# Performance work log

Hardware: AMD Instinct MI355X
Metric: run time of the kernel (lower is better)

## Reference

```python
import jax, jax.numpy as jnp
import numpy as np

N = 50000        # nodes
E = 1600000      # edges (before self loops)
IN = 256         # in_channels
C = 32           # hidden_channels (per head)
H = 4            # heads
OUT = 64         # out_channels
NEG_SLOPE = 0.2  # PyG GATConv default


def setup_inputs() -> dict:
    key = jax.random.key(0)
    ks = jax.random.split(key, 8)
    x = jax.random.normal(ks[0], (N, IN), dtype=jnp.float32)
    edge_index = jax.random.randint(ks[1], (2, E), 0, N, dtype=jnp.int64)
    s = 0.05
    W = jax.random.normal(ks[2], (IN, H * C), dtype=jnp.float32) * s
    att_src = jax.random.normal(ks[3], (H, C), dtype=jnp.float32) * s
    att_dst = jax.random.normal(ks[4], (H, C), dtype=jnp.float32) * s
    bias = jnp.zeros((H * C,), dtype=jnp.float32)
    lin_W = jax.random.normal(ks[5], (H * C, OUT), dtype=jnp.float32) * s
    lin_b = jnp.zeros((OUT,), dtype=jnp.float32)
    return {"x": x, "edge_index": edge_index, "W": W, "att_src": att_src,
            "att_dst": att_dst, "bias": bias, "lin_W": lin_W, "lin_b": lin_b}


def reference(x, edge_index, W, att_src, att_dst, bias, lin_W, lin_b):
    # Linear transform per head: [N, H, C]
    h = (x @ W).reshape(N, H, C)
    # Per-node attention halves (PyG GATConv): [N, H]
    a_src = jnp.einsum('nhc,hc->nh', h, att_src)
    a_dst = jnp.einsum('nhc,hc->nh', h, att_dst)
    # Add self loops (PyG default add_self_loops=True)
    loop = jnp.arange(N, dtype=edge_index.dtype)
    src = jnp.concatenate([edge_index[0], loop])  # message source j
    dst = jnp.concatenate([edge_index[1], loop])  # message target i
    # Edge attention logits: LeakyReLU(a_src[j] + a_dst[i])  -> [E+N, H]
    e = jax.nn.leaky_relu(a_src[src] + a_dst[dst], negative_slope=NEG_SLOPE)
    # Segment softmax over incoming edges of each destination node
    emax = jax.lax.stop_gradient(jax.ops.segment_max(e, dst, num_segments=N))
    emax = jnp.where(jnp.isfinite(emax), emax, 0.0)
    ex = jnp.exp(e - emax[dst])
    denom = jax.ops.segment_sum(ex, dst, num_segments=N)
    alpha = ex / denom[dst]  # [E+N, H]; self loops guarantee denom > 0
    # Weighted scatter-sum of source features: [N, H, C]
    msg = alpha[:, :, None] * h[src]
    agg = jax.ops.segment_sum(msg, dst, num_segments=N)
    out = agg.reshape(N, H * C) + bias  # concat heads + bias
    out = jax.nn.elu(out)
    return out @ lin_W + lin_b
```

## Files before the change

kernel.cpp:

```cpp
#include <hip/hip_runtime.h>
#include <cstdint>
#include <cstddef>

#define N_NODES 50000
#define N_EDGES 1600000
#define TOT_E   (N_EDGES + N_NODES)
#define IN_DIM  256
#define HC      128
#define NHEAD   4
#define OUT_DIM 64

#define SHIFT   7
#define BSZ     128
#define NBUK    ((N_NODES + BSZ - 1) / BSZ)
#define CHUNK   2048
#define EPT     8
#define NCHUNK  ((TOT_E + CHUNK - 1) / CHUNK)
#define CAP     6144

#define XPAD 264
#define HPAD 132

typedef __attribute__((ext_vector_type(8))) short bf16x8;
typedef __attribute__((ext_vector_type(4))) float f32x4;

static __device__ __forceinline__ uint16_t f2bf(float f) {
    uint32_t u = __float_as_uint(f);
    uint32_t r = (u + 0x7fffu + ((u >> 16) & 1u)) >> 16;
    return (uint16_t)r;
}
static __device__ __forceinline__ float bf_lo(uint32_t u) {
    return __uint_as_float(u << 16);
}
static __device__ __forceinline__ float bf_hi(uint32_t u) {
    return __uint_as_float(u & 0xffff0000u);
}

__global__ __launch_bounds__(256) void w2bf(const float* __restrict__ W,
                                            uint16_t* __restrict__ wt) {
    int idx = blockIdx.x * 256 + threadIdx.x;
    int n = idx >> 8, k = idx & 255;
    wt[idx] = f2bf(W[(size_t)k * HC + n]);
}

__global__ __launch_bounds__(256) void k1_mfma(const float* __restrict__ x,
                                               const uint16_t* __restrict__ wt,
                                               const float* __restrict__ att_src,
                                               const float* __restrict__ att_dst,
                                               uint16_t* __restrict__ hb,
                                               float* __restrict__ a_src,
                                               float* __restrict__ a_dst) {
    __shared__ char smem[64 * 528];
    __shared__ float att_s[HC], att_d[HC];
    uint16_t* xs = (uint16_t*)smem;
    float*    hs = (float*)smem;

    const int tid  = threadIdx.x;
    const int wave = tid >> 6;
    const int lane = tid & 63;
    const int m    = lane & 15;
    const int q    = lane >> 4;
    const int row0 = blockIdx.x * 64;

    if (tid < HC) { att_s[tid] = att_src[tid]; att_d[tid] = att_dst[tid]; }

    for (int i = tid * 4; i < 64 * IN_DIM; i += 1024) {
        int r = i >> 8, c = i & 255;
        int gr = row0 + r;
        float4 v = make_float4(0.f, 0.f, 0.f, 0.f);
        if (gr < N_NODES) v = *(const float4*)(x + (size_t)gr * IN_DIM + c);
        uint32_t lo = (uint32_t)f2bf(v.x) | ((uint32_t)f2bf(v.y) << 16);
        uint32_t hi = (uint32_t)f2bf(v.z) | ((uint32_t)f2bf(v.w) << 16);
        *(uint2*)(xs + r * XPAD + c) = make_uint2(lo, hi);
    }
    __syncthreads();

    f32x4 acc[8];
    #pragma unroll
    for (int t = 0; t < 8; ++t) acc[t] = (f32x4){0.f, 0.f, 0.f, 0.f};

    const int arow = wave * 16 + m;
    #pragma unroll
    for (int ks = 0; ks < IN_DIM; ks += 32) {
        bf16x8 a = *(const bf16x8*)(xs + arow * XPAD + ks + q * 8);
        #pragma unroll
        for (int t = 0; t < 8; ++t) {
            bf16x8 b = *(const bf16x8*)(wt + (size_t)(t * 16 + m) * IN_DIM + ks + q * 8);
            acc[t] = __builtin_amdgcn_mfma_f32_16x16x32_bf16(a, b, acc[t], 0, 0, 0);
        }
    }
    __syncthreads();

    #pragma unroll
    for (int t = 0; t < 8; ++t)
        #pragma unroll
        for (int r = 0; r < 4; ++r)
            hs[(wave * 16 + q * 4 + r) * HPAD + t * 16 + m] = acc[t][r];
    __syncthreads();

    for (int i = tid * 4; i < 64 * HC; i += 1024) {
        int r = i >> 7, c = i & 127;
        if (row0 + r < N_NODES) {
            float4 v = *(const float4*)(hs + r * HPAD + c);
            uint32_t lo = (uint32_t)f2bf(v.x) | ((uint32_t)f2bf(v.y) << 16);
            uint32_t hi = (uint32_t)f2bf(v.z) | ((uint32_t)f2bf(v.w) << 16);
            *(uint2*)(hb + (size_t)(row0 + r) * HC + c) = make_uint2(lo, hi);
        }
    }
    {
        int r = tid >> 2, hd = tid & 3;
        if (row0 + r < N_NODES) {
            float s = 0.f, d = 0.f;
            #pragma unroll
            for (int j = 0; j < 32; ++j) {
                float v = hs[r * HPAD + hd * 32 + j];
                s = fmaf(v, att_s[hd * 32 + j], s);
                d = fmaf(v, att_d[hd * 32 + j], d);
            }
            a_src[(row0 + r) * NHEAD + hd] = s;
            a_dst[(row0 + r) * NHEAD + hd] = d;
        }
    }
}

__global__ __launch_bounds__(256) void p3_bin(const int* __restrict__ ei,
                                              int* __restrict__ gcur,
                                              uint32_t* __restrict__ binned) {
    __shared__ int hist[NBUK];
    __shared__ int lcur[NBUK];
    const int tid = threadIdx.x;
    for (int i = tid; i < NBUK; i += 256) hist[i] = 0;
    __syncthreads();

    uint32_t wreg[EPT];
    const int base = blockIdx.x * CHUNK;
    #pragma unroll
    for (int k = 0; k < EPT; ++k) {
        int e = base + k * 256 + tid;
        uint32_t word = 0xFFFFFFFFu;
        if (e < TOT_E) {
            int src, dst;
            if (e < N_EDGES) { src = ei[e]; dst = ei[N_EDGES + e]; }
            else             { src = e - N_EDGES; dst = src; }
            int b = dst >> SHIFT;
            word = (uint32_t)src | ((uint32_t)(dst & (BSZ - 1)) << 16)
                 | ((uint32_t)b << 23);
            atomicAdd(&hist[b], 1);
        }
        wreg[k] = word;
    }
    __syncthreads();
    for (int i = tid; i < NBUK; i += 256) {
        int c = hist[i];
        lcur[i] = c ? atomicAdd(&gcur[i], c) : 0;
    }
    __syncthreads();
    #pragma unroll
    for (int k = 0; k < EPT; ++k) {
        uint32_t word = wreg[k];
        if (word != 0xFFFFFFFFu) {
            int b = (int)(word >> 23);
            int pos = atomicAdd(&lcur[b], 1);
            if (pos < CAP) binned[(size_t)b * CAP + pos] = word;
        }
    }
}

__global__ __launch_bounds__(512) void p4_csr(const uint32_t* __restrict__ binned,
                                              const int* __restrict__ gcur,
                                              int* __restrict__ rbeg,
                                              int* __restrict__ rend,
                                              int* __restrict__ csr_src) {
    __shared__ uint32_t ew[CAP];
    __shared__ int ncnt[BSZ];
    __shared__ int ncur[BSZ];
    __shared__ int wtot;
    const int b    = blockIdx.x;
    const int base = b * CAP;
    int cnt = gcur[b];
    if (cnt > CAP) cnt = CAP;
    const int tid  = threadIdx.x;

    if (tid < BSZ) ncnt[tid] = 0;
    __syncthreads();

    for (int i = tid; i < cnt; i += 512) {
        uint32_t word = binned[base + i];
        ew[i] = word;
        atomicAdd(&ncnt[(word >> 16) & (BSZ - 1)], 1);
    }
    __syncthreads();

    int v = 0, inc = 0;
    if (tid < BSZ) {
        v = ncnt[tid];
        inc = v;
        int lane = tid & 63;
        #pragma unroll
        for (int d = 1; d < 64; d <<= 1) {
            int t = __shfl_up(inc, d, 64);
            if (lane >= d) inc += t;
        }
        if (tid == 63) wtot = inc;
    }
    __syncthreads();
    if (tid < BSZ) {
        int ex = inc - v + ((tid >= 64) ? wtot : 0);
        int node = b * BSZ + tid;
        if (node < N_NODES) {
            rbeg[node] = base + ex;
            rend[node] = base + ex + v;
        }
        ncur[tid] = ex;
    }
    __syncthreads();

    for (int i = tid; i < cnt; i += 512) {
        uint32_t word = ew[i];
        int local = (word >> 16) & (BSZ - 1);
        int r = atomicAdd(&ncur[local], 1);
        csr_src[base + r] = (int)(word & 0xFFFFu);
    }
}

__global__ __launch_bounds__(64) void k6_agg(const uint32_t* __restrict__ hb32,
                                             const float* __restrict__ a_src,
                                             const float* __restrict__ a_dst,
                                             const int* __restrict__ rbeg,
                                             const int* __restrict__ rend,
                                             const int* __restrict__ csr_src,
                                             const float* __restrict__ bias,
                                             uint32_t* __restrict__ actb) {
    const int node = blockIdx.x;
    const int lane = threadIdx.x;
    const int head = lane >> 4;

    const float ad  = a_dst[node * NHEAD + head];
    const uint32_t* hbl = hb32 + lane;
    const float*    ash = a_src + head;

    int p   = rbeg[node];
    const int end = rend[node];

    float l = 0.f, acc0 = 0.f, acc1 = 0.f;

    for (; p + 4 <= end; p += 4) {
        int s0 = csr_src[p + 0];
        int s1 = csr_src[p + 1];
        int s2 = csr_src[p + 2];
        int s3 = csr_src[p + 3];
        float e0 = ash[s0 * NHEAD] + ad;
        float e1 = ash[s1 * NHEAD] + ad;
        float e2 = ash[s2 * NHEAD] + ad;
        float e3 = ash[s3 * NHEAD] + ad;
        uint32_t u0 = hbl[(size_t)s0 * 64];
        uint32_t u1 = hbl[(size_t)s1 * 64];
        uint32_t u2 = hbl[(size_t)s2 * 64];
        uint32_t u3 = hbl[(size_t)s3 * 64];
        e0 = fmaxf(e0, 0.2f * e0);
        e1 = fmaxf(e1, 0.2f * e1);
        e2 = fmaxf(e2, 0.2f * e2);
        e3 = fmaxf(e3, 0.2f * e3);
        float w0 = __expf(e0), w1 = __expf(e1);
        float w2 = __expf(e2), w3 = __expf(e3);
        l += (w0 + w1) + (w2 + w3);
        acc0 = fmaf(w0, bf_lo(u0), acc0);
        acc1 = fmaf(w0, bf_hi(u0), acc1);
        acc0 = fmaf(w1, bf_lo(u1), acc0);
        acc1 = fmaf(w1, bf_hi(u1), acc1);
        acc0 = fmaf(w2, bf_lo(u2), acc0);
        acc1 = fmaf(w2, bf_hi(u2), acc1);
        acc0 = fmaf(w3, bf_lo(u3), acc0);
        acc1 = fmaf(w3, bf_hi(u3), acc1);
    }
    for (; p < end; ++p) {
        int s = csr_src[p];
        float e = ash[s * NHEAD] + ad;
        e = fmaxf(e, 0.2f * e);
        float w = __expf(e);
        uint32_t u = hbl[(size_t)s * 64];
        l += w;
        acc0 = fmaf(w, bf_lo(u), acc0);
        acc1 = fmaf(w, bf_hi(u), acc1);
    }

    const int c0 = lane << 1;
    float inv = 1.f / l;
    float o0 = acc0 * inv + bias[c0];
    float o1 = acc1 * inv + bias[c0 + 1];
    o0 = (o0 > 0.f) ? o0 : (__expf(o0) - 1.f);
    o1 = (o1 > 0.f) ? o1 : (__expf(o1) - 1.f);
    actb[(size_t)node * 64 + lane] = (uint32_t)f2bf(o0) | ((uint32_t)f2bf(o1) << 16);
}

__global__ __launch_bounds__(512) void k7_out(const uint32_t* __restrict__ actb,
                                              const float* __restrict__ linW,
                                              const float* __restrict__ linb,
                                              float* __restrict__ out) {
    __shared__ float sW[HC * OUT_DIM];
    __shared__ float srow[32 * HC];
    const int tid   = threadIdx.x;
    const int node0 = blockIdx.x * 32;

    for (int i = tid * 4; i < HC * OUT_DIM; i += 512 * 4)
        *(float4*)(sW + i) = *(const float4*)(linW + i);
    {
        int i = tid * 4;
        int r = i >> 6, cw = i & 63;
        int node = node0 + r;
        uint4 v = make_uint4(0, 0, 0, 0);
        if (node < N_NODES) v = *(const uint4*)(actb + (size_t)node * 64 + cw);
        float* d = srow + r * HC + cw * 2;
        d[0] = bf_lo(v.x); d[1] = bf_hi(v.x);
        d[2] = bf_lo(v.y); d[3] = bf_hi(v.y);
        d[4] = bf_lo(v.z); d[5] = bf_hi(v.z);
        d[6] = bf_lo(v.w); d[7] = bf_hi(v.w);
    }
    __syncthreads();

    const int r    = tid >> 4;
    const int colb = (tid & 15) << 2;
    float4 acc = *(const float4*)(linb + colb);
    const float* rp = srow + r * HC;

    #pragma unroll
    for (int k = 0; k < HC; k += 4) {
        float4 xv = *(const float4*)(rp + k);
        float4 w0 = *(const float4*)(sW + (k + 0) * OUT_DIM + colb);
        float4 w1 = *(const float4*)(sW + (k + 1) * OUT_DIM + colb);
        float4 w2 = *(const float4*)(sW + (k + 2) * OUT_DIM + colb);
        float4 w3 = *(const float4*)(sW + (k + 3) * OUT_DIM + colb);
        acc.x += xv.x * w0.x; acc.x += xv.y * w1.x; acc.x += xv.z * w2.x; acc.x += xv.w * w3.x;
        acc.y += xv.x * w0.y; acc.y += xv.y * w1.y; acc.y += xv.z * w2.y; acc.y += xv.w * w3.y;
        acc.z += xv.x * w0.z; acc.z += xv.y * w1.z; acc.z += xv.z * w2.z; acc.z += xv.w * w3.z;
        acc.w += xv.x * w0.w; acc.w += xv.y * w1.w; acc.w += xv.z * w2.w; acc.w += xv.w * w3.w;
    }

    int node = node0 + r;
    if (node < N_NODES)
        *(float4*)(out + (size_t)node * OUT_DIM + colb) = acc;
}

extern "C" void kernel_launch(void* const* d_in, const int* in_sizes, int n_in,
                              void* d_out, int out_size, void* d_ws, size_t ws_size,
                              hipStream_t stream) {
    (void)in_sizes; (void)n_in; (void)out_size; (void)ws_size;
    const float* x       = (const float*)d_in[0];
    const int*   ei      = (const int*)d_in[1];
    const float* W       = (const float*)d_in[2];
    const float* att_src = (const float*)d_in[3];
    const float* att_dst = (const float*)d_in[4];
    const float* bias    = (const float*)d_in[5];
    const float* linW    = (const float*)d_in[6];
    const float* linb    = (const float*)d_in[7];
    float*       out     = (float*)d_out;

    char*  ws  = (char*)d_ws;
    size_t off = 0;
    auto alloc = [&](size_t bytes) -> void* {
        void* p = ws + off;
        off += (bytes + 255) & ~(size_t)255;
        return p;
    };
    uint16_t* hb     = (uint16_t*)alloc((size_t)N_NODES * HC * 2);
    uint16_t* wt     = (uint16_t*)alloc((size_t)HC * IN_DIM * 2);
    uint32_t* actb   = (uint32_t*)alloc((size_t)N_NODES * 64 * 4);
    float*    a_src  = (float*)alloc((size_t)N_NODES * NHEAD * 4);
    float*    a_dst  = (float*)alloc((size_t)N_NODES * NHEAD * 4);
    int*      gcur   = (int*)alloc((size_t)NBUK * 4);
    int*      rbeg   = (int*)alloc((size_t)N_NODES * 4);
    int*      rend   = (int*)alloc((size_t)N_NODES * 4);
    uint32_t* binned = (uint32_t*)alloc((size_t)NBUK * CAP * 4);
    int*      csr    = (int*)alloc((size_t)NBUK * CAP * 4);

    hipMemsetAsync(gcur, 0, (size_t)NBUK * 4, stream);

    w2bf<<<(HC * IN_DIM) / 256, 256, 0, stream>>>(W, wt);
    k1_mfma<<<(N_NODES + 63) / 64, 256, 0, stream>>>(x, wt, att_src, att_dst,
                                                     hb, a_src, a_dst);
    p3_bin<<<NCHUNK, 256, 0, stream>>>(ei, gcur, binned);
    p4_csr<<<NBUK, 512, 0, stream>>>(binned, gcur, rbeg, rend, csr);
    k6_agg<<<N_NODES, 64, 0, stream>>>((const uint32_t*)hb, a_src, a_dst,
                                       rbeg, rend, csr, bias, actb);
    k7_out<<<(N_NODES + 31) / 32, 512, 0, stream>>>(actb, linW, linb, out);
}
```

Measured before the change: 265.1 us.

## Fuse GEMM with edge binning and fold CSR build into aggregation

Folds the gcur memset into the weight conversion kernel and runs the MFMA projection and edge binning as two block ranges of one launch. The separate CSR kernel is removed: each aggregation block reads its bucket, keeps the edges for 32 destination nodes, counting-sorts them in shared memory, then aggregates with one wave per node in turn. This cuts launches and the global CSR write and read, but every bucket is scanned four times, and a quarter-bucket overflowing QCAP would silently drop edges.

```diff
diff --git a/kernel.cpp b/kernel.cpp
--- a/kernel.cpp
+++ b/kernel.cpp
@@ -17,9 +17,11 @@
 #define EPT     8
 #define NCHUNK  ((TOT_E + CHUNK - 1) / CHUNK)
 #define CAP     6144
+#define QCAP    1792
 
 #define XPAD 264
 #define HPAD 132
+#define K1_NB ((N_NODES + 63) / 64)
 
 typedef __attribute__((ext_vector_type(8))) short bf16x8;
 typedef __attribute__((ext_vector_type(4))) float f32x4;
@@ -37,260 +39,257 @@
 }
 
 __global__ __launch_bounds__(256) void w2bf(const float* __restrict__ W,
-                                            uint16_t* __restrict__ wt) {
+                                            uint16_t* __restrict__ wt,
+                                            int* __restrict__ gcur) {
     int idx = blockIdx.x * 256 + threadIdx.x;
     int n = idx >> 8, k = idx & 255;
     wt[idx] = f2bf(W[(size_t)k * HC + n]);
-}
-
-__global__ __launch_bounds__(256) void k1_mfma(const float* __restrict__ x,
-                                               const uint16_t* __restrict__ wt,
-                                               const float* __restrict__ att_src,
-                                               const float* __restrict__ att_dst,
-                                               uint16_t* __restrict__ hb,
-                                               float* __restrict__ a_src,
-                                               float* __restrict__ a_dst) {
+    if (idx < NBUK) gcur[idx] = 0;
+}
+
+__global__ __launch_bounds__(256) void k1p3(const float* __restrict__ x,
+                                            const uint16_t* __restrict__ wt,
+                                            const float* __restrict__ att_src,
+                                            const float* __restrict__ att_dst,
+                                            uint16_t* __restrict__ hb,
+                                            float* __restrict__ a_src,
+                                            float* __restrict__ a_dst,
+                                            const int* __restrict__ ei,
+                                            int* __restrict__ gcur,
+                                            uint32_t* __restrict__ binned) {
     __shared__ char smem[64 * 528];
     __shared__ float att_s[HC], att_d[HC];
-    uint16_t* xs = (uint16_t*)smem;
-    float*    hs = (float*)smem;
-
-    const int tid  = threadIdx.x;
+    const int tid = threadIdx.x;
+
+    if (blockIdx.x < K1_NB) {
+        uint16_t* xs = (uint16_t*)smem;
+        float*    hs = (float*)smem;
+        const int wave = tid >> 6;
+        const int lane = tid & 63;
+        const int m    = lane & 15;
+        const int q    = lane >> 4;
+        const int row0 = blockIdx.x * 64;
+
+        if (tid < HC) { att_s[tid] = att_src[tid]; att_d[tid] = att_dst[tid]; }
+
+        for (int i = tid * 4; i < 64 * IN_DIM; i += 1024) {
+            int r = i >> 8, c = i & 255;
+            int gr = row0 + r;
+            float4 v = make_float4(0.f, 0.f, 0.f, 0.f);
+            if (gr < N_NODES) v = *(const float4*)(x + (size_t)gr * IN_DIM + c);
+            uint32_t lo = (uint32_t)f2bf(v.x) | ((uint32_t)f2bf(v.y) << 16);
+            uint32_t hi = (uint32_t)f2bf(v.z) | ((uint32_t)f2bf(v.w) << 16);
+            *(uint2*)(xs + r * XPAD + c) = make_uint2(lo, hi);
+        }
+        __syncthreads();
+
+        f32x4 acc[8];
+        #pragma unroll
+        for (int t = 0; t < 8; ++t) acc[t] = (f32x4){0.f, 0.f, 0.f, 0.f};
+
+        const int arow = wave * 16 + m;
+        #pragma unroll
+        for (int ks = 0; ks < IN_DIM; ks += 32) {
+            bf16x8 a = *(const bf16x8*)(xs + arow * XPAD + ks + q * 8);
+            #pragma unroll
+            for (int t = 0; t < 8; ++t) {
+                bf16x8 b = *(const bf16x8*)(wt + (size_t)(t * 16 + m) * IN_DIM + ks + q * 8);
+                acc[t] = __builtin_amdgcn_mfma_f32_16x16x32_bf16(a, b, acc[t], 0, 0, 0);
+            }
+        }
+        __syncthreads();
+
+        #pragma unroll
+        for (int t = 0; t < 8; ++t)
+            #pragma unroll
+            for (int r = 0; r < 4; ++r)
+                hs[(wave * 16 + q * 4 + r) * HPAD + t * 16 + m] = acc[t][r];
+        __syncthreads();
+
+        for (int i = tid * 4; i < 64 * HC; i += 1024) {
+            int r = i >> 7, c = i & 127;
+            if (row0 + r < N_NODES) {
+                float4 v = *(const float4*)(hs + r * HPAD + c);
+                uint32_t lo = (uint32_t)f2bf(v.x) | ((uint32_t)f2bf(v.y) << 16);
+                uint32_t hi = (uint32_t)f2bf(v.z) | ((uint32_t)f2bf(v.w) << 16);
+                *(uint2*)(hb + (size_t)(row0 + r) * HC + c) = make_uint2(lo, hi);
+            }
+        }
+        {
+            int r = tid >> 2, hd = tid & 3;
+            if (row0 + r < N_NODES) {
+                float s = 0.f, d = 0.f;
+                #pragma unroll
+                for (int j = 0; j < 32; ++j) {
+                    float v = hs[r * HPAD + hd * 32 + j];
+                    s = fmaf(v, att_s[hd * 32 + j], s);
+                    d = fmaf(v, att_d[hd * 32 + j], d);
+                }
+                a_src[(row0 + r) * NHEAD + hd] = s;
+                a_dst[(row0 + r) * NHEAD + hd] = d;
+            }
+        }
+    } else {
+        int* hist = (int*)smem;
+        int* lcur = hist + NBUK;
+        for (int i = tid; i < NBUK; i += 256) hist[i] = 0;
+        __syncthreads();
+
+        uint32_t wreg[EPT];
+        const int base = (blockIdx.x - K1_NB) * CHUNK;
+        #pragma unroll
+        for (int k = 0; k < EPT; ++k) {
+            int e = base + k * 256 + tid;
+            uint32_t word = 0xFFFFFFFFu;
+            if (e < TOT_E) {
+                int src, dst;
+                if (e < N_EDGES) { src = ei[e]; dst = ei[N_EDGES + e]; }
+                else             { src = e - N_EDGES; dst = src; }
+                int b = dst >> SHIFT;
+                word = (uint32_t)src | ((uint32_t)(dst & (BSZ - 1)) << 16)
+                     | ((uint32_t)b << 23);
+                atomicAdd(&hist[b], 1);
+            }
+            wreg[k] = word;
+        }
+        __syncthreads();
+        for (int i = tid; i < NBUK; i += 256) {
+            int c = hist[i];
+            lcur[i] = c ? atomicAdd(&gcur[i], c) : 0;
+        }
+        __syncthreads();
+        #pragma unroll
+        for (int k = 0; k < EPT; ++k) {
+            uint32_t word = wreg[k];
+            if (word != 0xFFFFFFFFu) {
+                int b = (int)(word >> 23);
+                int pos = atomicAdd(&lcur[b], 1);
+                if (pos < CAP) binned[(size_t)b * CAP + pos] = word;
+            }
+        }
+    }
+}
+
+__global__ __launch_bounds__(256) void q4_agg(const uint32_t* __restrict__ binned,
+                                              const int* __restrict__ gcur,
+                                              const uint32_t* __restrict__ hb32,
+                                              const float* __restrict__ a_src,
+                                              const float* __restrict__ a_dst,
+                                              const float* __restrict__ bias,
+                                              uint32_t* __restrict__ actb) {
+    __shared__ uint32_t ewb[QCAP];
+    __shared__ uint32_t ew2[QCAP];
+    __shared__ int ncnt[32], nbeg[32], ncur[32];
+    __shared__ int tot;
+    const int b   = blockIdx.x >> 2;
+    const int sub = blockIdx.x & 3;
+    const int tid = threadIdx.x;
+
+    int cnt = gcur[b];
+    if (cnt > CAP) cnt = CAP;
+    if (tid == 0) tot = 0;
+    if (tid < 32) ncnt[tid] = 0;
+    __syncthreads();
+
+    const uint32_t* bb = binned + (size_t)b * CAP;
+    for (int i = tid; i < cnt; i += 256) {
+        uint32_t word = bb[i];
+        int dl = (word >> 16) & 127;
+        if ((dl >> 5) == sub) {
+            int pos = atomicAdd(&tot, 1);
+            if (pos < QCAP) ewb[pos] = word;
+            atomicAdd(&ncnt[dl & 31], 1);
+        }
+    }
+    __syncthreads();
+    int T = tot;
+    if (T > QCAP) T = QCAP;
+
+    if (tid < 32) {
+        int v = ncnt[tid];
+        int inc = v;
+        #pragma unroll
+        for (int d = 1; d < 32; d <<= 1) {
+            int t = __shfl_up(inc, d, 64);
+            if (tid >= d) inc += t;
+        }
+        nbeg[tid] = inc - v;
+        ncur[tid] = inc - v;
+    }
+    __syncthreads();
+    for (int i = tid; i < T; i += 256) {
+        uint32_t word = ewb[i];
+        int ln  = (word >> 16) & 31;
+        int pos = atomicAdd(&ncur[ln], 1);
+        ew2[pos] = word & 0xFFFFu;
+    }
+    __syncthreads();
+
     const int wave = tid >> 6;
     const int lane = tid & 63;
-    const int m    = lane & 15;
-    const int q    = lane >> 4;
-    const int row0 = blockIdx.x * 64;
-
-    if (tid < HC) { att_s[tid] = att_src[tid]; att_d[tid] = att_dst[tid]; }
-
-    for (int i = tid * 4; i < 64 * IN_DIM; i += 1024) {
-        int r = i >> 8, c = i & 255;
-        int gr = row0 + r;
-        float4 v = make_float4(0.f, 0.f, 0.f, 0.f);
-        if (gr < N_NODES) v = *(const float4*)(x + (size_t)gr * IN_DIM + c);
-        uint32_t lo = (uint32_t)f2bf(v.x) | ((uint32_t)f2bf(v.y) << 16);
-        uint32_t hi = (uint32_t)f2bf(v.z) | ((uint32_t)f2bf(v.w) << 16);
-        *(uint2*)(xs + r * XPAD + c) = make_uint2(lo, hi);
-    }
-    __syncthreads();
-
-    f32x4 acc[8];
-    #pragma unroll
-    for (int t = 0; t < 8; ++t) acc[t] = (f32x4){0.f, 0.f, 0.f, 0.f};
-
-    const int arow = wave * 16 + m;
-    #pragma unroll
-    for (int ks = 0; ks < IN_DIM; ks += 32) {
-        bf16x8 a = *(const bf16x8*)(xs + arow * XPAD + ks + q * 8);
-        #pragma unroll
-        for (int t = 0; t < 8; ++t) {
-            bf16x8 b = *(const bf16x8*)(wt + (size_t)(t * 16 + m) * IN_DIM + ks + q * 8);
-            acc[t] = __builtin_amdgcn_mfma_f32_16x16x32_bf16(a, b, acc[t], 0, 0, 0);
-        }
-    }
-    __syncthreads();
-
-    #pragma unroll
-    for (int t = 0; t < 8; ++t)
-        #pragma unroll
-        for (int r = 0; r < 4; ++r)
-            hs[(wave * 16 + q * 4 + r) * HPAD + t * 16 + m] = acc[t][r];
-    __syncthreads();
-
-    for (int i = tid * 4; i < 64 * HC; i += 1024) {
-        int r = i >> 7, c = i & 127;
-        if (row0 + r < N_NODES) {
-            float4 v = *(const float4*)(hs + r * HPAD + c);
-            uint32_t lo = (uint32_t)f2bf(v.x) | ((uint32_t)f2bf(v.y) << 16);
-            uint32_t hi = (uint32_t)f2bf(v.z) | ((uint32_t)f2bf(v.w) << 16);
-            *(uint2*)(hb + (size_t)(row0 + r) * HC + c) = make_uint2(lo, hi);
-        }
-    }
-    {
-        int r = tid >> 2, hd = tid & 3;
-        if (row0 + r < N_NODES) {
-            float s = 0.f, d = 0.f;
-            #pragma unroll
-            for (int j = 0; j < 32; ++j) {
-                float v = hs[r * HPAD + hd * 32 + j];
-                s = fmaf(v, att_s[hd * 32 + j], s);
-                d = fmaf(v, att_d[hd * 32 + j], d);
-            }
-            a_src[(row0 + r) * NHEAD + hd] = s;
-            a_dst[(row0 + r) * NHEAD + hd] = d;
-        }
-    }
-}
-
-__global__ __launch_bounds__(256) void p3_bin(const int* __restrict__ ei,
-                                              int* __restrict__ gcur,
-                                              uint32_t* __restrict__ binned) {
-    __shared__ int hist[NBUK];
-    __shared__ int lcur[NBUK];
-    const int tid = threadIdx.x;
-    for (int i = tid; i < NBUK; i += 256) hist[i] = 0;
-    __syncthreads();
-
-    uint32_t wreg[EPT];
-    const int base = blockIdx.x * CHUNK;
-    #pragma unroll
-    for (int k = 0; k < EPT; ++k) {
-        int e = base + k * 256 + tid;
-        uint32_t word = 0xFFFFFFFFu;
-        if (e < TOT_E) {
-            int src, dst;
-            if (e < N_EDGES) { src = ei[e]; dst = ei[N_EDGES + e]; }
-            else             { src = e - N_EDGES; dst = src; }
-            int b = dst >> SHIFT;
-            word = (uint32_t)src | ((uint32_t)(dst & (BSZ - 1)) << 16)
-                 | ((uint32_t)b << 23);
-            atomicAdd(&hist[b], 1);
-        }
-        wreg[k] = word;
-    }
-    __syncthreads();
-    for (int i = tid; i < NBUK; i += 256) {
-        int c = hist[i];
-        lcur[i] = c ? atomicAdd(&gcur[i], c) : 0;
-    }
-    __syncthreads();
-    #pragma unroll
-    for (int k = 0; k < EPT; ++k) {
-        uint32_t word = wreg[k];
-        if (word != 0xFFFFFFFFu) {
-            int b = (int)(word >> 23);
-            int pos = atomicAdd(&lcur[b], 1);
-            if (pos < CAP) binned[(size_t)b * CAP + pos] = word;
-        }
-    }
-}
-
-__global__ __launch_bounds__(512) void p4_csr(const uint32_t* __restrict__ binned,
-                                              const int* __restrict__ gcur,
-                                              int* __restrict__ rbeg,
-                                              int* __restrict__ rend,
-                                              int* __restrict__ csr_src) {
-    __shared__ uint32_t ew[CAP];
-    __shared__ int ncnt[BSZ];
-    __shared__ int ncur[BSZ];
-    __shared__ int wtot;
-    const int b    = blockIdx.x;
-    const int base = b * CAP;
-    int cnt = gcur[b];
-    if (cnt > CAP) cnt = CAP;
-    const int tid  = threadIdx.x;
-
-    if (tid < BSZ) ncnt[tid] = 0;
-    __syncthreads();
-
-    for (int i = tid; i < cnt; i += 512) {
-        uint32_t word = binned[base + i];
-        ew[i] = word;
-        atomicAdd(&ncnt[(word >> 16) & (BSZ - 1)], 1);
-    }
-    __syncthreads();
-
-    int v = 0, inc = 0;
-    if (tid < BSZ) {
-        v = ncnt[tid];
-        inc = v;
-        int lane = tid & 63;
-        #pragma unroll
-        for (int d = 1; d < 64; d <<= 1) {
-            int t = __shfl_up(inc, d, 64);
-            if (lane >= d) inc += t;
-        }
-        if (tid == 63) wtot = inc;
-    }
-    __syncthreads();
-    if (tid < BSZ) {
-        int ex = inc - v + ((tid >= 64) ? wtot : 0);
-        int node = b * BSZ + tid;
-        if (node < N_NODES) {
-            rbeg[node] = base + ex;
-            rend[node] = base + ex + v;
-        }
-        ncur[tid] = ex;
-    }
-    __syncthreads();
-
-    for (int i = tid; i < cnt; i += 512) {
-        uint32_t word = ew[i];
-        int local = (word >> 16) & (BSZ - 1);
-        int r = atomicAdd(&ncur[local], 1);
-        csr_src[base + r] = (int)(word & 0xFFFFu);
-    }
-}
-
-__global__ __launch_bounds__(64) void k6_agg(const uint32_t* __restrict__ hb32,
-                                             const float* __restrict__ a_src,
-                                             const float* __restrict__ a_dst,
-                                             const int* __restrict__ rbeg,
-                                             const int* __restrict__ rend,
-                                             const int* __restrict__ csr_src,
-                                             const float* __restrict__ bias,
-                                             uint32_t* __restrict__ actb) {
-    const int node = blockIdx.x;
-    const int lane = threadIdx.x;
     const int head = lane >> 4;
-
-    const float ad  = a_dst[node * NHEAD + head];
     const uint32_t* hbl = hb32 + lane;
     const float*    ash = a_src + head;
 
-    int p   = rbeg[node];
-    const int end = rend[node];
-
-    float l = 0.f, acc0 = 0.f, acc1 = 0.f;
-
-    for (; p + 4 <= end; p += 4) {
-        int s0 = csr_src[p + 0];
-        int s1 = csr_src[p + 1];
-        int s2 = csr_src[p + 2];
-        int s3 = csr_src[p + 3];
-        float e0 = ash[s0 * NHEAD] + ad;
-        float e1 = ash[s1 * NHEAD] + ad;
-        float e2 = ash[s2 * NHEAD] + ad;
-        float e3 = ash[s3 * NHEAD] + ad;
-        uint32_t u0 = hbl[(size_t)s0 * 64];
-        uint32_t u1 = hbl[(size_t)s1 * 64];
-        uint32_t u2 = hbl[(size_t)s2 * 64];
-        uint32_t u3 = hbl[(size_t)s3 * 64];
-        e0 = fmaxf(e0, 0.2f * e0);
-        e1 = fmaxf(e1, 0.2f * e1);
-        e2 = fmaxf(e2, 0.2f * e2);
-        e3 = fmaxf(e3, 0.2f * e3);
-        float w0 = __expf(e0), w1 = __expf(e1);
-        float w2 = __expf(e2), w3 = __expf(e3);
-        l += (w0 + w1) + (w2 + w3);
-        acc0 = fmaf(w0, bf_lo(u0), acc0);
-        acc1 = fmaf(w0, bf_hi(u0), acc1);
-        acc0 = fmaf(w1, bf_lo(u1), acc0);
-        acc1 = fmaf(w1, bf_hi(u1), acc1);
-        acc0 = fmaf(w2, bf_lo(u2), acc0);
-        acc1 = fmaf(w2, bf_hi(u2), acc1);
-        acc0 = fmaf(w3, bf_lo(u3), acc0);
-        acc1 = fmaf(w3, bf_hi(u3), acc1);
-    }
-    for (; p < end; ++p) {
-        int s = csr_src[p];
-        float e = ash[s * NHEAD] + ad;
-        e = fmaxf(e, 0.2f * e);
-        float w = __expf(e);
-        uint32_t u = hbl[(size_t)s * 64];
-        l += w;
-        acc0 = fmaf(w, bf_lo(u), acc0);
-        acc1 = fmaf(w, bf_hi(u), acc1);
-    }
-
-    const int c0 = lane << 1;
-    float inv = 1.f / l;
-    float o0 = acc0 * inv + bias[c0];
-    float o1 = acc1 * inv + bias[c0 + 1];
-    o0 = (o0 > 0.f) ? o0 : (__expf(o0) - 1.f);
-    o1 = (o1 > 0.f) ? o1 : (__expf(o1) - 1.f);
-    actb[(size_t)node * 64 + lane] = (uint32_t)f2bf(o0) | ((uint32_t)f2bf(o1) << 16);
+    for (int k = 0; k < 8; ++k) {
+        const int ln   = wave * 8 + k;
+        const int node = b * BSZ + sub * 32 + ln;
+        if (node >= N_NODES) continue;
+
+        const float ad = a_dst[node * NHEAD + head];
+        int p = nbeg[ln];
+        const int end = p + ncnt[ln];
+
+        float l = 0.f, acc0 = 0.f, acc1 = 0.f;
+
+        for (; p + 4 <= end; p += 4) {
+            int s0 = (int)ew2[p + 0];
+            int s1 = (int)ew2[p + 1];
+            int s2 = (int)ew2[p + 2];
+            int s3 = (int)ew2[p + 3];
+            float e0 = ash[s0 * NHEAD] + ad;
+            float e1 = ash[s1 * NHEAD] + ad;
+            float e2 = ash[s2 * NHEAD] + ad;
+            float e3 = ash[s3 * NHEAD] + ad;
+            uint32_t u0 = hbl[(size_t)s0 * 64];
+            uint32_t u1 = hbl[(size_t)s1 * 64];
+            uint32_t u2 = hbl[(size_t)s2 * 64];
+            uint32_t u3 = hbl[(size_t)s3 * 64];
+            e0 = fmaxf(e0, 0.2f * e0);
+            e1 = fmaxf(e1, 0.2f * e1);
+            e2 = fmaxf(e2, 0.2f * e2);
+            e3 = fmaxf(e3, 0.2f * e3);
+            float w0 = __expf(e0), w1 = __expf(e1);
+            float w2 = __expf(e2), w3 = __expf(e3);
+            l += (w0 + w1) + (w2 + w3);
+            acc0 = fmaf(w0, bf_lo(u0), acc0);
+            acc1 = fmaf(w0, bf_hi(u0), acc1);
+            acc0 = fmaf(w1, bf_lo(u1), acc0);
+            acc1 = fmaf(w1, bf_hi(u1), acc1);
+            acc0 = fmaf(w2, bf_lo(u2), acc0);
+            acc1 = fmaf(w2, bf_hi(u2), acc1);
+            acc0 = fmaf(w3, bf_lo(u3), acc0);
+            acc1 = fmaf(w3, bf_hi(u3), acc1);
+        }
+        for (; p < end; ++p) {
+            int s = (int)ew2[p];
+            float e = ash[s * NHEAD] + ad;
+            e = fmaxf(e, 0.2f * e);
+            float w = __expf(e);
+            uint32_t u = hbl[(size_t)s * 64];
+            l += w;
+            acc0 = fmaf(w, bf_lo(u), acc0);
+            acc1 = fmaf(w, bf_hi(u), acc1);
+        }
+
+        const int c0 = lane << 1;
+        float inv = 1.f / l;
+        float o0 = acc0 * inv + bias[c0];
+        float o1 = acc1 * inv + bias[c0 + 1];
+        o0 = (o0 > 0.f) ? o0 : (__expf(o0) - 1.f);
+        o1 = (o1 > 0.f) ? o1 : (__expf(o1) - 1.f);
+        actb[(size_t)node * 64 + lane] = (uint32_t)f2bf(o0) | ((uint32_t)f2bf(o1) << 16);
+    }
 }
 
 __global__ __launch_bounds__(512) void k7_out(const uint32_t* __restrict__ actb,
@@ -368,19 +367,13 @@
     float*    a_src  = (float*)alloc((size_t)N_NODES * NHEAD * 4);
     float*    a_dst  = (float*)alloc((size_t)N_NODES * NHEAD * 4);
     int*      gcur   = (int*)alloc((size_t)NBUK * 4);
-    int*      rbeg   = (int*)alloc((size_t)N_NODES * 4);
-    int*      rend   = (int*)alloc((size_t)N_NODES * 4);
     uint32_t* binned = (uint32_t*)alloc((size_t)NBUK * CAP * 4);
-    int*      csr    = (int*)alloc((size_t)NBUK * CAP * 4);
-
-    hipMemsetAsync(gcur, 0, (size_t)NBUK * 4, stream);
-
-    w2bf<<<(HC * IN_DIM) / 256, 256, 0, stream>>>(W, wt);
-    k1_mfma<<<(N_NODES + 63) / 64, 256, 0, stream>>>(x, wt, att_src, att_dst,
-                                                     hb, a_src, a_dst);
-    p3_bin<<<NCHUNK, 256, 0, stream>>>(ei, gcur, binned);
-    p4_csr<<<NBUK, 512, 0, stream>>>(binned, gcur, rbeg, rend, csr);
-    k6_agg<<<N_NODES, 64, 0, stream>>>((const uint32_t*)hb, a_src, a_dst,
-                                       rbeg, rend, csr, bias, actb);
+
+    w2bf<<<(HC * IN_DIM) / 256, 256, 0, stream>>>(W, wt, gcur);
+    k1p3<<<K1_NB + NCHUNK, 256, 0, stream>>>(x, wt, att_src, att_dst,
+                                             hb, a_src, a_dst,
+                                             ei, gcur, binned);
+    q4_agg<<<NBUK * 4, 256, 0, stream>>>(binned, gcur, (const uint32_t*)hb,
+                                         a_src, a_dst, bias, actb);
     k7_out<<<(N_NODES + 31) / 32, 512, 0, stream>>>(actb, linW, linb, out);
 }
```

Result: faster. 244.5 us (-7.8%).
